# Kernel optimization log

Hardware: AMD Instinct MI355X
Metric: run time of the kernel (lower is better)

Reference implementation:

```python
import jax, jax.numpy as jnp
import numpy as np

N, B, C, IC = 4096, 4, 64, 32  # seq len, batch, in_channels, inter_channels
BN_EPS = 1e-5


def setup_inputs() -> dict:
    key = jax.random.key(0)
    ks = jax.random.split(key, 12)
    s = 0.05
    return {
        "x_thisBranch": jax.random.normal(ks[0], (N, B, C), jnp.float32),
        "x_otherBranch": jax.random.normal(ks[1], (N, B, C), jnp.float32),
        "g_w": jax.random.normal(ks[2], (IC, C), jnp.float32) * s,
        "g_b": jax.random.normal(ks[3], (IC,), jnp.float32) * s,
        "theta_w": jax.random.normal(ks[4], (IC, C), jnp.float32) * s,
        "theta_b": jax.random.normal(ks[5], (IC,), jnp.float32) * s,
        "phi_w": jax.random.normal(ks[6], (IC, C), jnp.float32) * s,
        "phi_b": jax.random.normal(ks[7], (IC,), jnp.float32) * s,
        "wz_w": jax.random.normal(ks[8], (C, IC), jnp.float32) * s,
        "wz_b": jax.random.normal(ks[9], (C,), jnp.float32) * s,
        "bn_gamma": jax.random.normal(ks[10], (C,), jnp.float32) * s + 1.0,
        "bn_beta": jax.random.normal(ks[11], (C,), jnp.float32) * s,
    }


def reference(x_thisBranch, x_otherBranch, g_w, g_b, theta_w, theta_b,
              phi_w, phi_b, wz_w, wz_b, bn_gamma, bn_beta):
    # [N,B,C] -> [B,C,N] as in torch permute(1,2,0)
    xt = jnp.transpose(x_thisBranch, (1, 2, 0))   # (B,C,N)
    xo = jnp.transpose(x_otherBranch, (1, 2, 0))  # (B,C,N)

    # 1x1 conv1d == per-position linear over channels
    g_x = jnp.einsum('ic,bcn->bni', g_w, xt) + g_b            # (B,N,IC)
    theta_x = jnp.einsum('ic,bcn->bin', theta_w, xt) + theta_b[:, None]  # (B,IC,N)
    phi_x = jnp.einsum('ic,bcn->bni', phi_w, xo) + phi_b      # (B,N,IC)

    # f = phi_x @ theta_x : rows indexed by other-branch positions
    f = jnp.einsum('bni,bim->bnm', phi_x, theta_x)            # (B,N,N)
    a = jax.nn.softmax(f, axis=-1)                            # embedded mode

    y = jnp.einsum('bnm,bmi->bni', a, g_x)                    # (B,N,IC)
    y = jnp.transpose(y, (0, 2, 1))                           # (B,IC,N)

    # W_z: 1x1 conv + BatchNorm1d (training-mode batch stats)
    wy = jnp.einsum('ci,bin->bcn', wz_w, y) + wz_b[:, None]   # (B,C,N)
    mean = wy.mean(axis=(0, 2), keepdims=True)
    var = wy.var(axis=(0, 2), keepdims=True)
    wy = (wy - mean) / jnp.sqrt(var + BN_EPS) * bn_gamma[:, None] + bn_beta[:, None]

    return wy + xt
```

## Files before the change

kernel.cpp:

```cpp
#include <hip/hip_runtime.h>
#include <hip/hip_bf16.h>
#include <math.h>

typedef unsigned short ushort_t;
typedef __attribute__((ext_vector_type(8))) short short8;
typedef __attribute__((ext_vector_type(4))) float float4v;
typedef __attribute__((ext_vector_type(16))) float float16v;

#define NN 4096
#define BB 4
#define CC 64
#define ICH 32

#define OFF_QB 0
#define OFF_KB 262144
#define OFF_VT 524288
#define OFF_OP 786432

static __device__ __forceinline__ ushort_t f2b(float f) {
  union { float f; unsigned u; } v;
  v.f = f;
  return (ushort_t)((v.u + 0x8000u) >> 16);
}
static __device__ __forceinline__ unsigned pack2(float x, float y) {
  return (unsigned)f2b(x) | ((unsigned)f2b(y) << 16);
}
static __device__ __forceinline__ short8 cvt8lds(const float* p) {
  short8 r;
#pragma unroll
  for (int j = 0; j < 8; j++) r[j] = (short)f2b(p[j]);
  return r;
}

__global__ __launch_bounds__(256) void proj_kernel(
    const float* __restrict__ xt, const float* __restrict__ xo,
    const float* __restrict__ gw, const float* __restrict__ gb,
    const float* __restrict__ tw, const float* __restrict__ tb,
    const float* __restrict__ pw, const float* __restrict__ pb,
    ushort_t* __restrict__ Qb, ushort_t* __restrict__ Kb,
    ushort_t* __restrict__ Vt) {
  __shared__ float xls[64 * 68];
  __shared__ float wls[ICH * 68];
  __shared__ float bls[ICH];
  __shared__ ushort_t ol[2304];

  int t = threadIdx.x;
  int wv = t >> 6, lane = t & 63, l15 = lane & 15, quad = lane >> 4;
  int b = blockIdx.y, z = blockIdx.z;
  int n0 = blockIdx.x * 64;

  const float* xsrc = (z == 1) ? xo : xt;
  const float* W = (z == 0) ? tw : (z == 1) ? pw : gw;
  const float* Bv = (z == 0) ? tb : (z == 1) ? pb : gb;

#pragma unroll
  for (int it = 0; it < 4; it++) {
    int lin = it * 256 + t;
    int row = lin >> 4, seg = lin & 15;
    float4 v = *(const float4*)(xsrc + ((size_t)(n0 + row) * BB + b) * CC + seg * 4);
    *(float4*)(xls + row * 68 + seg * 4) = v;
  }
#pragma unroll
  for (int it = 0; it < 2; it++) {
    int lin = it * 256 + t;
    int row = lin >> 4, seg = lin & 15;
    float4 v = *(const float4*)(W + (size_t)row * CC + seg * 4);
    *(float4*)(wls + row * 68 + seg * 4) = v;
  }
  if (t < ICH) bls[t] = Bv[t];
  __syncthreads();

  const float* xr = xls + (wv * 16 + l15) * 68;
  short8 a0 = cvt8lds(xr + quad * 8);
  short8 a1 = cvt8lds(xr + 32 + quad * 8);

#pragma unroll
  for (int h = 0; h < 2; h++) {
    int i = h * 16 + l15;
    short8 b0 = cvt8lds(wls + i * 68 + quad * 8);
    short8 b1 = cvt8lds(wls + i * 68 + 32 + quad * 8);
    float bias = bls[i];
    float4v acc = {bias, bias, bias, bias};
    acc = __builtin_amdgcn_mfma_f32_16x16x32_bf16(a0, b0, acc, 0, 0, 0);
    acc = __builtin_amdgcn_mfma_f32_16x16x32_bf16(a1, b1, acc, 0, 0, 0);
    if (z < 2) {
#pragma unroll
      for (int r = 0; r < 4; r++)
        ol[(wv * 16 + quad * 4 + r) * 36 + i] = f2b(acc[r]);
    } else {
#pragma unroll
      for (int r = 0; r < 4; r++)
        ol[i * 68 + wv * 16 + quad * 4 + r] = f2b(acc[r]);
    }
  }
  __syncthreads();

  if (z < 2) {
    ushort_t* dst = (z == 0) ? Kb : Qb;
    int row = t >> 2, seg = t & 3;
    short8 v;
#pragma unroll
    for (int k = 0; k < 8; k++) v[k] = (short)ol[row * 36 + seg * 8 + k];
    *(short8*)(dst + ((size_t)b * NN + n0 + row) * ICH + seg * 8) = v;
  } else {
    int i = t & 31, seg = t >> 5;
    short8 v;
#pragma unroll
    for (int k = 0; k < 8; k++) v[k] = (short)ol[i * 68 + seg * 8 + k];
    *(short8*)(Vt + (size_t)(b * ICH + i) * NN + n0 + seg * 8) = v;
  }
}

__global__ __launch_bounds__(256) void attn_kernel(
    const ushort_t* __restrict__ Qb, const ushort_t* __restrict__ Kb,
    const ushort_t* __restrict__ Vt, float* __restrict__ OPT,
    float* __restrict__ LS, int splits) {
  int t = threadIdx.x;
  int wv = t >> 6, lane = t & 63;
  int l31 = lane & 31, h = lane >> 5;
  int s = blockIdx.y, b = blockIdx.z;
  int q0 = blockIdx.x * 256 + wv * 64;
  int kspan = NN / splits;
  int mbeg = s * kspan, mend = mbeg + kspan;

  const ushort_t* Kbb = Kb + (size_t)b * NN * ICH;
  const ushort_t* Vtb = Vt + (size_t)b * ICH * NN;

  short8 bq0[2], bq1[2];
#pragma unroll
  for (int f = 0; f < 2; f++) {
    const ushort_t* qp = Qb + ((size_t)b * NN + q0 + f * 32 + l31) * ICH + h * 8;
    bq0[f] = *(const short8*)(qp);
    bq1[f] = *(const short8*)(qp + 16);
  }

  float16v ot[2];
#pragma unroll
  for (int f = 0; f < 2; f++)
#pragma unroll
    for (int r = 0; r < 16; r++) ot[f][r] = 0.f;
  float lsp[2] = {0.f, 0.f};

  for (int m0 = mbeg; m0 < mend; m0 += 32) {
    const ushort_t* kp = Kbb + (size_t)(m0 + l31) * ICH + h * 8;
    short8 ka0 = *(const short8*)(kp);
    short8 ka1 = *(const short8*)(kp + 16);
    const ushort_t* vp = Vtb + (size_t)l31 * NN + m0 + h * 8;
    short8 va0 = *(const short8*)(vp);
    short8 va1 = *(const short8*)(vp + 16);

#pragma unroll
    for (int f = 0; f < 2; f++) {
      float16v st;
#pragma unroll
      for (int r = 0; r < 16; r++) st[r] = 0.f;
      st = __builtin_amdgcn_mfma_f32_32x32x16_bf16(ka0, bq0[f], st, 0, 0, 0);
      st = __builtin_amdgcn_mfma_f32_32x32x16_bf16(ka1, bq1[f], st, 0, 0, 0);

      float p[16];
#pragma unroll
      for (int r = 0; r < 16; r++) {
        p[r] = __expf(st[r]);
        lsp[f] += p[r];
      }
      unsigned dw[8];
#pragma unroll
      for (int j = 0; j < 8; j++) dw[j] = pack2(p[2 * j], p[2 * j + 1]);

      unsigned send0 = h ? dw[0] : dw[2];
      unsigned send1 = h ? dw[1] : dw[3];
      unsigned r0 = (unsigned)__shfl_xor((int)send0, 32, 64);
      unsigned r1 = (unsigned)__shfl_xor((int)send1, 32, 64);
      union { unsigned u[4]; short8 s8; } b1u;
      b1u.u[0] = h ? r0 : dw[0];
      b1u.u[1] = h ? r1 : dw[1];
      b1u.u[2] = h ? dw[2] : r0;
      b1u.u[3] = h ? dw[3] : r1;
      unsigned send2 = h ? dw[4] : dw[6];
      unsigned send3 = h ? dw[5] : dw[7];
      unsigned r2 = (unsigned)__shfl_xor((int)send2, 32, 64);
      unsigned r3 = (unsigned)__shfl_xor((int)send3, 32, 64);
      union { unsigned u[4]; short8 s8; } b2u;
      b2u.u[0] = h ? r2 : dw[4];
      b2u.u[1] = h ? r3 : dw[5];
      b2u.u[2] = h ? dw[6] : r2;
      b2u.u[3] = h ? dw[7] : r3;

      ot[f] = __builtin_amdgcn_mfma_f32_32x32x16_bf16(va0, b1u.s8, ot[f], 0, 0, 0);
      ot[f] = __builtin_amdgcn_mfma_f32_32x32x16_bf16(va1, b2u.s8, ot[f], 0, 0, 0);
    }
  }

  size_t bs = (size_t)(b * splits + s);
#pragma unroll
  for (int f = 0; f < 2; f++) {
    float v = lsp[f];
    v += __shfl_xor(v, 32, 64);
    if (h == 0) LS[bs * NN + q0 + f * 32 + l31] = v;
#pragma unroll
    for (int r = 0; r < 16; r++) {
      int ch = (r & 3) + 8 * (r >> 2) + 4 * h;
      OPT[(bs * ICH + ch) * NN + q0 + f * 32 + l31] = ot[f][r];
    }
  }
}

__global__ __launch_bounds__(256) void wz_kernel(
    const float* __restrict__ OPT, const float* __restrict__ LS,
    const float* __restrict__ wz_w, const float* __restrict__ wz_b,
    float* __restrict__ WY, float* __restrict__ SP, int splits) {
  __shared__ float yl[64 * 36];
  __shared__ float lsum[64];
  __shared__ float red1[256], red2[256];

  int b = blockIdx.y, n0 = blockIdx.x * 64, t = threadIdx.x;
  int blkid = b * 64 + blockIdx.x;

  if (t < 64) {
    float ssum = 0.f;
    for (int sp = 0; sp < splits; sp++)
      ssum += LS[(size_t)(b * splits + sp) * NN + n0 + t];
    lsum[t] = ssum;
  }
  __syncthreads();
#pragma unroll
  for (int it = 0; it < 8; it++) {
    int lin = it * 256 + t;
    int i = lin >> 6, dn = lin & 63;
    float sacc = 0.f;
    for (int sp = 0; sp < splits; sp++)
      sacc += OPT[((size_t)(b * splits + sp) * ICH + i) * NN + n0 + dn];
    yl[dn * 36 + i] = sacc / lsum[dn];
  }
  __syncthreads();

  int c = t >> 2, sub = t & 3;
  float4 w4[8];
#pragma unroll
  for (int j = 0; j < 8; j++) w4[j] = ((const float4*)(wz_w + c * ICH))[j];
  float bc = wz_b[c];
  float s1 = 0.f, s2 = 0.f;
#pragma unroll
  for (int d = 0; d < 16; d++) {
    int dn = sub * 16 + d;
    const float4* y4 = (const float4*)(yl + dn * 36);
    float acc = bc;
#pragma unroll
    for (int j = 0; j < 8; j++) {
      float4 y = y4[j];
      acc += w4[j].x * y.x + w4[j].y * y.y + w4[j].z * y.z + w4[j].w * y.w;
    }
    WY[((size_t)(b * CC + c)) * NN + n0 + dn] = acc;
    s1 += acc;
    s2 += acc * acc;
  }
  red1[t] = s1;
  red2[t] = s2;
  __syncthreads();
  if (t < 64) {
    float a1 = red1[t * 4] + red1[t * 4 + 1] + red1[t * 4 + 2] + red1[t * 4 + 3];
    float a2 = red2[t * 4] + red2[t * 4 + 1] + red2[t * 4 + 2] + red2[t * 4 + 3];
    SP[(size_t)blkid * 64 + t] = a1;
    SP[16384 + (size_t)blkid * 64 + t] = a2;
  }
}

__global__ __launch_bounds__(256) void norm_kernel(
    const float* __restrict__ SP, const float* __restrict__ gamma,
    const float* __restrict__ beta, const float* __restrict__ WY,
    const float* __restrict__ xthis, float* __restrict__ out) {
  __shared__ double rd1[256], rd2[256];
  __shared__ float abr[128];
  __shared__ float xl[64 * 65];
  int b = blockIdx.y, n0 = blockIdx.x * 64, t = threadIdx.x;

  {
    int cc = t & 63, part = t >> 6;
    double d1 = 0.0, d2 = 0.0;
    for (int k = part * 64; k < part * 64 + 64; k++) {
      d1 += (double)SP[(size_t)k * 64 + cc];
      d2 += (double)SP[16384 + (size_t)k * 64 + cc];
    }
    rd1[t] = d1;
    rd2[t] = d2;
  }
#pragma unroll
  for (int it = 0; it < 16; it++) {
    int lin = it * 256 + t;
    int c = lin & 63, dn = lin >> 6;
    xl[dn * 65 + c] = xthis[((size_t)(n0 + dn) * BB + b) * CC + c];
  }
  __syncthreads();
  if (t < 64) {
    double a1 = rd1[t] + rd1[64 + t] + rd1[128 + t] + rd1[192 + t];
    double a2 = rd2[t] + rd2[64 + t] + rd2[128 + t] + rd2[192 + t];
    double inv = 1.0 / (double)(BB * NN);
    double mean = a1 * inv;
    double var = a2 * inv - mean * mean;
    if (var < 0.0) var = 0.0;
    double rstd = 1.0 / sqrt(var + 1e-5);
    float A = gamma[t] * (float)rstd;
    abr[t] = A;
    abr[64 + t] = beta[t] - (float)mean * A;
  }
  __syncthreads();
#pragma unroll
  for (int it = 0; it < 16; it++) {
    int lin = it * 256 + t;
    int c = lin >> 6, dn = lin & 63;
    size_t idx = ((size_t)(b * CC + c)) * NN + n0 + dn;
    out[idx] = WY[idx] * abr[c] + abr[64 + c] + xl[dn * 65 + c];
  }
}

extern "C" void kernel_launch(void* const* d_in, const int* in_sizes, int n_in,
                              void* d_out, int out_size, void* d_ws,
                              size_t ws_size, hipStream_t stream) {
  const float* x_this = (const float*)d_in[0];
  const float* x_other = (const float*)d_in[1];
  const float* g_w = (const float*)d_in[2];
  const float* g_b = (const float*)d_in[3];
  const float* th_w = (const float*)d_in[4];
  const float* th_b = (const float*)d_in[5];
  const float* ph_w = (const float*)d_in[6];
  const float* ph_b = (const float*)d_in[7];
  const float* wz_w = (const float*)d_in[8];
  const float* wz_b = (const float*)d_in[9];
  const float* gamma = (const float*)d_in[10];
  const float* beta = (const float*)d_in[11];
  float* out = (float*)d_out;

  float* ws = (float*)d_ws;
  ushort_t* Qb = (ushort_t*)(ws + OFF_QB);
  ushort_t* Kb = (ushort_t*)(ws + OFF_KB);
  ushort_t* Vt = (ushort_t*)(ws + OFF_VT);

  int splits = 8;
  while (splits > 1 &&
         ws_size < (size_t)(786432 + (size_t)splits * 540672 + 32768 +
                            1048576) * 4)
    splits >>= 1;
  float* OPT = ws + OFF_OP;
  float* LS = OPT + (size_t)splits * 524288;
  float* SP = LS + (size_t)splits * 16384;
  float* WY = SP + 32768;

  hipLaunchKernelGGL(proj_kernel, dim3(NN / 64, BB, 3), dim3(256), 0, stream,
                     x_this, x_other, g_w, g_b, th_w, th_b, ph_w, ph_b,
                     Qb, Kb, Vt);
  hipLaunchKernelGGL(attn_kernel, dim3(NN / 256, splits, BB), dim3(256), 0,
                     stream, Qb, Kb, Vt, OPT, LS, splits);
  hipLaunchKernelGGL(wz_kernel, dim3(NN / 64, BB), dim3(256), 0, stream,
                     OPT, LS, wz_w, wz_b, WY, SP, splits);
  hipLaunchKernelGGL(norm_kernel, dim3(NN / 64, BB), dim3(256), 0, stream,
                     SP, gamma, beta, WY, x_this, out);
}
```

Measured before the change: 151.0 us.

## Fuse W_z projection into attention kernel with in-block key-split reduction

The attention kernel now launches 512-thread blocks. Each of the 8 waves handles the same 64 queries over a different 512-key span. The partial outputs and row sums are reduced through shared memory instead of being written to global OPT/LS buffers, and the W_z projection and per-block BN partial statistics are computed in the same kernel. This removes one kernel launch and the global round-trip of the split partial results, at the cost of 256 blocks versus 512 before and a heavier shared-memory footprint per block.

```diff
diff --git a/kernel.cpp b/kernel.cpp
--- a/kernel.cpp
+++ b/kernel.cpp
@@ -11,11 +11,13 @@
 #define BB 4
 #define CC 64
 #define ICH 32
+#define KSPAN 512
 
 #define OFF_QB 0
 #define OFF_KB 262144
 #define OFF_VT 524288
-#define OFF_OP 786432
+#define OFF_WY 786432
+#define OFF_SP 1835008
 
 static __device__ __forceinline__ ushort_t f2b(float f) {
   union { float f; unsigned u; } v;
@@ -111,20 +113,31 @@
   }
 }
 
-__global__ __launch_bounds__(256) void attn_kernel(
+__global__ __launch_bounds__(512) void attn_kernel(
     const ushort_t* __restrict__ Qb, const ushort_t* __restrict__ Kb,
-    const ushort_t* __restrict__ Vt, float* __restrict__ OPT,
-    float* __restrict__ LS, int splits) {
+    const ushort_t* __restrict__ Vt, const float* __restrict__ wz_w,
+    const float* __restrict__ wz_b, float* __restrict__ WY,
+    float* __restrict__ SP) {
+  __shared__ float pot[4][ICH][72];
+  __shared__ float pls[8][64];
+  __shared__ float wzl[CC * ICH];
+  __shared__ float bls[CC];
+  __shared__ float yl[64 * 36];
+  __shared__ float lsum[64];
+
   int t = threadIdx.x;
-  int wv = t >> 6, lane = t & 63;
+  int w = t >> 6, lane = t & 63;
   int l31 = lane & 31, h = lane >> 5;
-  int s = blockIdx.y, b = blockIdx.z;
-  int q0 = blockIdx.x * 256 + wv * 64;
-  int kspan = NN / splits;
-  int mbeg = s * kspan, mend = mbeg + kspan;
+  int b = blockIdx.y;
+  int q0 = blockIdx.x * 64;
+  int blkid = b * 64 + blockIdx.x;
+
+  for (int l = t; l < CC * ICH; l += 512) wzl[l] = wz_w[l];
+  if (t < CC) bls[t] = wz_b[t];
 
   const ushort_t* Kbb = Kb + (size_t)b * NN * ICH;
   const ushort_t* Vtb = Vt + (size_t)b * ICH * NN;
+  int mbeg = w * KSPAN;
 
   short8 bq0[2], bq1[2];
 #pragma unroll
@@ -141,7 +154,9 @@
     for (int r = 0; r < 16; r++) ot[f][r] = 0.f;
   float lsp[2] = {0.f, 0.f};
 
-  for (int m0 = mbeg; m0 < mend; m0 += 32) {
+#pragma unroll 2
+  for (int c = 0; c < KSPAN / 32; c++) {
+    int m0 = mbeg + c * 32;
     const ushort_t* kp = Kbb + (size_t)(m0 + l31) * ICH + h * 8;
     short8 ka0 = *(const short8*)(kp);
     short8 ka1 = *(const short8*)(kp + 16);
@@ -191,58 +206,65 @@
     }
   }
 
-  size_t bs = (size_t)(b * splits + s);
+  float lv[2];
 #pragma unroll
   for (int f = 0; f < 2; f++) {
     float v = lsp[f];
     v += __shfl_xor(v, 32, 64);
-    if (h == 0) LS[bs * NN + q0 + f * 32 + l31] = v;
-#pragma unroll
-    for (int r = 0; r < 16; r++) {
-      int ch = (r & 3) + 8 * (r >> 2) + 4 * h;
-      OPT[(bs * ICH + ch) * NN + q0 + f * 32 + l31] = ot[f][r];
-    }
-  }
-}
-
-__global__ __launch_bounds__(256) void wz_kernel(
-    const float* __restrict__ OPT, const float* __restrict__ LS,
-    const float* __restrict__ wz_w, const float* __restrict__ wz_b,
-    float* __restrict__ WY, float* __restrict__ SP, int splits) {
-  __shared__ float yl[64 * 36];
-  __shared__ float lsum[64];
-  __shared__ float red1[256], red2[256];
-
-  int b = blockIdx.y, n0 = blockIdx.x * 64, t = threadIdx.x;
-  int blkid = b * 64 + blockIdx.x;
+    lv[f] = v;
+  }
+
+  if (w < 4) {
+#pragma unroll
+    for (int f = 0; f < 2; f++)
+#pragma unroll
+      for (int r = 0; r < 16; r++) {
+        int ch = (r & 3) + 8 * (r >> 2) + 4 * h;
+        pot[w][ch][f * 32 + l31] = ot[f][r];
+      }
+  }
+  if (h == 0) {
+#pragma unroll
+    for (int f = 0; f < 2; f++) pls[w][f * 32 + l31] = lv[f];
+  }
+  __syncthreads();
+  if (w >= 4) {
+#pragma unroll
+    for (int f = 0; f < 2; f++)
+#pragma unroll
+      for (int r = 0; r < 16; r++) {
+        int ch = (r & 3) + 8 * (r >> 2) + 4 * h;
+        pot[w - 4][ch][f * 32 + l31] += ot[f][r];
+      }
+  }
+  __syncthreads();
 
   if (t < 64) {
-    float ssum = 0.f;
-    for (int sp = 0; sp < splits; sp++)
-      ssum += LS[(size_t)(b * splits + sp) * NN + n0 + t];
-    lsum[t] = ssum;
-  }
-  __syncthreads();
-#pragma unroll
-  for (int it = 0; it < 8; it++) {
-    int lin = it * 256 + t;
+    float s = 0.f;
+#pragma unroll
+    for (int ww = 0; ww < 8; ww++) s += pls[ww][t];
+    lsum[t] = s;
+  }
+  __syncthreads();
+
+#pragma unroll
+  for (int k = 0; k < 4; k++) {
+    int lin = k * 512 + t;
     int i = lin >> 6, dn = lin & 63;
-    float sacc = 0.f;
-    for (int sp = 0; sp < splits; sp++)
-      sacc += OPT[((size_t)(b * splits + sp) * ICH + i) * NN + n0 + dn];
+    float sacc = pot[0][i][dn] + pot[1][i][dn] + pot[2][i][dn] + pot[3][i][dn];
     yl[dn * 36 + i] = sacc / lsum[dn];
   }
   __syncthreads();
 
-  int c = t >> 2, sub = t & 3;
+  int c = t >> 3, sub = t & 7;
   float4 w4[8];
 #pragma unroll
-  for (int j = 0; j < 8; j++) w4[j] = ((const float4*)(wz_w + c * ICH))[j];
-  float bc = wz_b[c];
+  for (int j = 0; j < 8; j++) w4[j] = ((const float4*)(wzl + c * ICH))[j];
+  float bc = bls[c];
   float s1 = 0.f, s2 = 0.f;
 #pragma unroll
-  for (int d = 0; d < 16; d++) {
-    int dn = sub * 16 + d;
+  for (int d = 0; d < 8; d++) {
+    int dn = sub * 8 + d;
     const float4* y4 = (const float4*)(yl + dn * 36);
     float acc = bc;
 #pragma unroll
@@ -250,18 +272,19 @@
       float4 y = y4[j];
       acc += w4[j].x * y.x + w4[j].y * y.y + w4[j].z * y.z + w4[j].w * y.w;
     }
-    WY[((size_t)(b * CC + c)) * NN + n0 + dn] = acc;
+    WY[((size_t)(b * CC + c)) * NN + q0 + dn] = acc;
     s1 += acc;
     s2 += acc * acc;
   }
-  red1[t] = s1;
-  red2[t] = s2;
-  __syncthreads();
-  if (t < 64) {
-    float a1 = red1[t * 4] + red1[t * 4 + 1] + red1[t * 4 + 2] + red1[t * 4 + 3];
-    float a2 = red2[t * 4] + red2[t * 4 + 1] + red2[t * 4 + 2] + red2[t * 4 + 3];
-    SP[(size_t)blkid * 64 + t] = a1;
-    SP[16384 + (size_t)blkid * 64 + t] = a2;
+  s1 += __shfl_xor(s1, 1, 64);
+  s2 += __shfl_xor(s2, 1, 64);
+  s1 += __shfl_xor(s1, 2, 64);
+  s2 += __shfl_xor(s2, 2, 64);
+  s1 += __shfl_xor(s1, 4, 64);
+  s2 += __shfl_xor(s2, 4, 64);
+  if (sub == 0) {
+    SP[(size_t)blkid * 64 + c] = s1;
+    SP[16384 + (size_t)blkid * 64 + c] = s2;
   }
 }
 
@@ -334,24 +357,14 @@
   ushort_t* Qb = (ushort_t*)(ws + OFF_QB);
   ushort_t* Kb = (ushort_t*)(ws + OFF_KB);
   ushort_t* Vt = (ushort_t*)(ws + OFF_VT);
-
-  int splits = 8;
-  while (splits > 1 &&
-         ws_size < (size_t)(786432 + (size_t)splits * 540672 + 32768 +
-                            1048576) * 4)
-    splits >>= 1;
-  float* OPT = ws + OFF_OP;
-  float* LS = OPT + (size_t)splits * 524288;
-  float* SP = LS + (size_t)splits * 16384;
-  float* WY = SP + 32768;
+  float* WY = ws + OFF_WY;
+  float* SP = ws + OFF_SP;
 
   hipLaunchKernelGGL(proj_kernel, dim3(NN / 64, BB, 3), dim3(256), 0, stream,
                      x_this, x_other, g_w, g_b, th_w, th_b, ph_w, ph_b,
                      Qb, Kb, Vt);
-  hipLaunchKernelGGL(attn_kernel, dim3(NN / 256, splits, BB), dim3(256), 0,
-                     stream, Qb, Kb, Vt, OPT, LS, splits);
-  hipLaunchKernelGGL(wz_kernel, dim3(NN / 64, BB), dim3(256), 0, stream,
-                     OPT, LS, wz_w, wz_b, WY, SP, splits);
+  hipLaunchKernelGGL(attn_kernel, dim3(NN / 64, BB), dim3(512), 0, stream,
+                     Qb, Kb, Vt, wz_w, wz_b, WY, SP);
   hipLaunchKernelGGL(norm_kernel, dim3(NN / 64, BB), dim3(256), 0, stream,
                      SP, gamma, beta, WY, x_this, out);
 }
```

Result: faster. 131.5 us (-12.9%).
